# Kernel optimization log

Hardware: AMD Instinct MI355X
Metric: run time of the kernel (lower is better)

Reference implementation:

```python
import jax, jax.numpy as jnp
import numpy as np

N_EMB = 512
EMB_DIM = 64
DECAY = 0.99
EPS = 1e-5


def setup_inputs() -> dict:
    key = jax.random.key(0)
    k1, k2 = jax.random.split(key)
    x = jax.random.normal(k1, (32, EMB_DIM, 64, 64), dtype=jnp.float32)
    weight = jax.random.uniform(k2, (EMB_DIM, N_EMB), dtype=jnp.float32)  # rd_init=True: torch.rand(emb_dim, n_emb)
    cluster_size = jnp.zeros((N_EMB,), dtype=jnp.float32)
    embed_avg = weight  # buffer initialized as embed.clone()
    return {"x": x, "weight": weight, "cluster_size": cluster_size, "embed_avg": embed_avg}


def reference(x, weight, cluster_size, embed_avg):
    B, D, H, W = x.shape
    n_emb = weight.shape[1]
    # (B, D, H, W) -> (N, D) tokens
    flat = jnp.transpose(x, (0, 2, 3, 1)).reshape(-1, D)
    dist = (jnp.sum(flat * flat, axis=1, keepdims=True)
            - 2.0 * (flat @ weight)
            + jnp.sum(weight * weight, axis=0)[None, :])
    argmin = jnp.argmin(dist, axis=1)                      # (N,)
    quant = jnp.take(weight.T, argmin, axis=0)             # gather -> (N, D)
    result = jnp.transpose(quant.reshape(B, H, W, D), (0, 3, 1, 2))  # (B, D, H, W)

    # --- EMA codebook update (training branch) ---
    ones = jnp.ones(argmin.shape, dtype=x.dtype)
    n_idx = jax.ops.segment_sum(ones, argmin, num_segments=n_emb)    # onehot.sum(0)
    n_idx = jnp.where(n_idx == 0, jnp.ones_like(n_idx), n_idx)       # clamp empty clusters to 1
    new_cluster_size = DECAY * cluster_size + (1.0 - DECAY) * n_idx
    embed_sum = jax.ops.segment_sum(flat, argmin, num_segments=n_emb).T  # flatten.T @ onehot -> (D, n_emb)
    new_embed_avg = DECAY * embed_avg + (1.0 - DECAY) * embed_sum
    n = jnp.sum(new_cluster_size)
    cs = (new_cluster_size + EPS) / (n + n_emb * EPS) * n
    new_weight = new_embed_avg / cs[None, :]

    return result, argmin.reshape(B, H, W), new_weight, new_cluster_size, new_embed_avg
```

## Files before the change

### kernel.cpp

```cpp
#include <hip/hip_runtime.h>

#define NEMB 512
#define EMB 64
#define BSTR 262144
#define DECAYF 0.99f
#define OMDF 0.01f
#define EPSF 1e-5f
#define GAP_T 0.012f
#define QCAP 32768

typedef __attribute__((ext_vector_type(8))) short bf16x8;
typedef __attribute__((ext_vector_type(4))) float f32x4;

__device__ __forceinline__ unsigned short f2bf(float f) {
    unsigned u = __float_as_uint(f);
    return (unsigned short)((u + 0x7FFFu + ((u >> 16) & 1u)) >> 16);
}
__device__ __forceinline__ float bf2f(unsigned short h) {
    return __uint_as_float(((unsigned)h) << 16);
}

__global__ void prep_kernel(const float* __restrict__ w,
                            unsigned short* __restrict__ wh, unsigned short* __restrict__ wl,
                            float* __restrict__ wsq,
                            float* __restrict__ cnt_ws, unsigned* __restrict__ gcnt) {
    int j = threadIdx.x;
    if (blockIdx.x < 8) {
        int d0 = blockIdx.x << 3;
        bf16x8 hb, lb;
#pragma unroll
        for (int i = 0; i < 8; ++i) {
            float v = w[(d0 + i) * NEMB + j];
            unsigned short h = f2bf(v);
            hb[i] = (short)h;
            lb[i] = (short)f2bf(v - bf2f(h));
        }
        *(bf16x8*)(wh + j * EMB + d0) = hb;
        *(bf16x8*)(wl + j * EMB + d0) = lb;
    } else {
        float s = 0.f;
#pragma unroll
        for (int d = 0; d < EMB; ++d) { float v = w[d * NEMB + j]; s = fmaf(v, v, s); }
        wsq[j] = s;
        cnt_ws[j] = 0.f;
        if (j == 0) *gcnt = 0u;
    }
}

#define UPD(S1, J1, S2, J2, s_, j_) do { \
    if (s_ < S1 || (s_ == S1 && j_ < J1)) { S2 = S1; J2 = J1; S1 = s_; J1 = j_; } \
    else if (s_ < S2 || (s_ == S2 && j_ < J2)) { S2 = s_; J2 = j_; } } while (0)

__global__ __launch_bounds__(512, 4) void vq_main(
    const float* __restrict__ x,
    const unsigned short* __restrict__ wh, const unsigned short* __restrict__ wl,
    const float* __restrict__ wsq,
    float* __restrict__ out_arg, unsigned* __restrict__ gcnt, int* __restrict__ queue)
{
    __shared__ __align__(16) unsigned char ubuf[65536];
    __shared__ float wsq_s[NEMB];
    __shared__ float xsq_s[256];

    float* xt = (float*)ubuf;
    unsigned short* whs = (unsigned short*)ubuf;
    unsigned short* wls = whs + 16384;

    const int tid = threadIdx.x;
    const int blk = blockIdx.x;
    const int b    = blk >> 4;
    const int hgrp = blk & 15;
    const int t0 = b * 4096 + hgrp * 256;
    const float* xbase = x + b * BSTR + hgrp * 256;

#pragma unroll
    for (int it = 0; it < 8; ++it) {
        int idx = tid + (it << 9);
        int d = idx >> 6, q = idx & 63;
        *(float4*)(xt + d * 256 + (q << 2)) = *(const float4*)(xbase + d * 4096 + (q << 2));
    }
    wsq_s[tid] = wsq[tid];
    __syncthreads();

    if (tid < 256) {
        float s = 0.f;
#pragma unroll
        for (int d = 0; d < EMB; ++d) { float v = xt[d * 256 + tid]; s = fmaf(v, v, s); }
        xsq_s[tid] = s;
    }

    const int lane = tid & 63;
    const int wave = tid >> 6;
    const int l15  = lane & 15;
    const int quad = lane >> 4;
    const int wbase = wave << 5;

    bf16x8 ah[2][2], al[2][2];
#pragma unroll
    for (int mt = 0; mt < 2; ++mt) {
        int m = wbase + (mt << 4) + l15;
#pragma unroll
        for (int ks = 0; ks < 2; ++ks) {
            int k0 = (ks << 5) + (quad << 3);
            bf16x8 hh, ll;
#pragma unroll
            for (int i = 0; i < 8; ++i) {
                float v = xt[(k0 + i) * 256 + m];
                unsigned short h = f2bf(v);
                hh[i] = (short)h;
                ll[i] = (short)f2bf(v - bf2f(h));
            }
            ah[mt][ks] = hh; al[mt][ks] = ll;
        }
    }
    __syncthreads();

    float xq[2][4];
#pragma unroll
    for (int mt = 0; mt < 2; ++mt)
#pragma unroll
        for (int r = 0; r < 4; ++r)
            xq[mt][r] = xsq_s[wbase + (mt << 4) + (quad << 2) + r];

    float v1[2][4], v2[2][4];
    int   j1[2][4];
#pragma unroll
    for (int mt = 0; mt < 2; ++mt)
#pragma unroll
        for (int r = 0; r < 4; ++r) { v1[mt][r] = 3.4e38f; v2[mt][r] = 3.4e38f; j1[mt][r] = 0; }

    const int m7 = l15 & 7;
    const int s0off = ((quad ^ m7) << 3);
    const int s1off = (((4 | quad) ^ m7) << 3);

    for (int half = 0; half < 2; ++half) {
#pragma unroll
        for (int it = 0; it < 8; ++it) {
            int e = tid + (it << 9);
            int arr  = e >> 11;
            int win  = e & 2047;
            int row  = win >> 3;
            int slot = win & 7;
            const unsigned short* src =
                (arr ? wl : wh) + ((half << 8) + row) * EMB + (slot << 3);
            bf16x8 v = *(const bf16x8*)src;
            unsigned short* dstb = arr ? wls : whs;
            *(bf16x8*)(dstb + row * EMB + ((slot ^ (row & 7)) << 3)) = v;
        }
        __syncthreads();

        const int nbase = half << 8;
#pragma unroll 2
        for (int it = 0; it < 16; ++it) {
            const int ib = ((it << 4) + l15) << 6;
            bf16x8 b0 = *(const bf16x8*)(whs + ib + s0off);
            bf16x8 b1 = *(const bf16x8*)(whs + ib + s1off);
            bf16x8 b2 = *(const bf16x8*)(wls + ib + s0off);
            bf16x8 b3 = *(const bf16x8*)(wls + ib + s1off);
            const int n = nbase + (it << 4) + l15;
            float wq = wsq_s[n];

            f32x4 acc0 = (f32x4){0.f, 0.f, 0.f, 0.f};
            f32x4 acc1 = (f32x4){0.f, 0.f, 0.f, 0.f};
            acc0 = __builtin_amdgcn_mfma_f32_16x16x32_bf16(ah[0][0], b0, acc0, 0, 0, 0);
            acc1 = __builtin_amdgcn_mfma_f32_16x16x32_bf16(ah[1][0], b0, acc1, 0, 0, 0);
            acc0 = __builtin_amdgcn_mfma_f32_16x16x32_bf16(ah[0][1], b1, acc0, 0, 0, 0);
            acc1 = __builtin_amdgcn_mfma_f32_16x16x32_bf16(ah[1][1], b1, acc1, 0, 0, 0);
            acc0 = __builtin_amdgcn_mfma_f32_16x16x32_bf16(ah[0][0], b2, acc0, 0, 0, 0);
            acc1 = __builtin_amdgcn_mfma_f32_16x16x32_bf16(ah[1][0], b2, acc1, 0, 0, 0);
            acc0 = __builtin_amdgcn_mfma_f32_16x16x32_bf16(ah[0][1], b3, acc0, 0, 0, 0);
            acc1 = __builtin_amdgcn_mfma_f32_16x16x32_bf16(ah[1][1], b3, acc1, 0, 0, 0);
            acc0 = __builtin_amdgcn_mfma_f32_16x16x32_bf16(al[0][0], b0, acc0, 0, 0, 0);
            acc1 = __builtin_amdgcn_mfma_f32_16x16x32_bf16(al[1][0], b0, acc1, 0, 0, 0);
            acc0 = __builtin_amdgcn_mfma_f32_16x16x32_bf16(al[0][1], b1, acc0, 0, 0, 0);
            acc1 = __builtin_amdgcn_mfma_f32_16x16x32_bf16(al[1][1], b1, acc1, 0, 0, 0);

#pragma unroll
            for (int r = 0; r < 4; ++r) {
                float s0 = fmaf(-2.f, acc0[r], xq[0][r] + wq);
                bool p0 = s0 < v1[0][r];
                float mx0 = fmaxf(s0, v1[0][r]);
                v1[0][r] = fminf(s0, v1[0][r]);
                v2[0][r] = fminf(v2[0][r], mx0);
                j1[0][r] = p0 ? n : j1[0][r];

                float s1 = fmaf(-2.f, acc1[r], xq[1][r] + wq);
                bool p1 = s1 < v1[1][r];
                float mx1 = fmaxf(s1, v1[1][r]);
                v1[1][r] = fminf(s1, v1[1][r]);
                v2[1][r] = fminf(v2[1][r], mx1);
                j1[1][r] = p1 ? n : j1[1][r];
            }
        }
        __syncthreads();
    }

#pragma unroll
    for (int mt = 0; mt < 2; ++mt)
#pragma unroll
        for (int r = 0; r < 4; ++r) {
            float a1 = v1[mt][r], a2 = v2[mt][r];
            int   aj = j1[mt][r];
#pragma unroll
            for (int msk = 1; msk < 16; msk <<= 1) {
                float o1 = __shfl_xor(a1, msk, 64);
                int   oj = __shfl_xor(aj, msk, 64);
                float o2 = __shfl_xor(a2, msk, 64);
                bool take = (o1 < a1) || (o1 == a1 && oj < aj);
                float mx = fmaxf(a1, o1);
                a2 = fminf(fminf(a2, o2), mx);
                a1 = fminf(a1, o1);
                aj = take ? oj : aj;
            }
            v1[mt][r] = a1; v2[mt][r] = a2; j1[mt][r] = aj;
        }

    if (l15 == 0) {
#pragma unroll
        for (int mt = 0; mt < 2; ++mt)
#pragma unroll
            for (int r = 0; r < 4; ++r) {
                int gt = t0 + wbase + (mt << 4) + (quad << 2) + r;
                out_arg[gt] = (float)j1[mt][r];
                if (v2[mt][r] - v1[mt][r] < GAP_T) {
                    unsigned idx = atomicAdd(gcnt, 1u);
                    if (idx < QCAP) queue[idx] = gt;
                }
            }
    }
}

__global__ __launch_bounds__(256) void refine_kernel(
    const float* __restrict__ x, const float* __restrict__ w,
    const float* __restrict__ wsq, const unsigned* __restrict__ gcnt,
    const int* __restrict__ queue, float* __restrict__ out_arg)
{
    __shared__ float wsq_s[NEMB];
    const int tid = threadIdx.x;
    wsq_s[tid] = wsq[tid];
    wsq_s[tid + 256] = wsq[tid + 256];
    __syncthreads();

    unsigned nfu = *gcnt;
    const int nf = (int)(nfu < (unsigned)QCAP ? nfu : (unsigned)QCAP);
    const int lane = tid & 63;
    const int gw = (blockIdx.x << 2) + (tid >> 6);

    for (int i = gw; i < nf; i += 1024) {
        const int t = queue[i] & 131071;
        const int b = t >> 12, pos = t & 4095;
        float xd = x[b * BSTR + lane * 4096 + pos];
        float xqv = xd * xd;
#pragma unroll
        for (int mk = 1; mk < 64; mk <<= 1) xqv += __shfl_xor(xqv, mk, 64);

        float accv[8];
#pragma unroll
        for (int k = 0; k < 8; ++k) accv[k] = 0.f;
#pragma unroll 4
        for (int d = 0; d < EMB; ++d) {
            float4 wa = *(const float4*)(w + d * NEMB + (lane << 2));
            float4 wb = *(const float4*)(w + d * NEMB + 256 + (lane << 2));
            float xv = __shfl(xd, d, 64);
            accv[0] = fmaf(xv, wa.x, accv[0]);
            accv[1] = fmaf(xv, wa.y, accv[1]);
            accv[2] = fmaf(xv, wa.z, accv[2]);
            accv[3] = fmaf(xv, wa.w, accv[3]);
            accv[4] = fmaf(xv, wb.x, accv[4]);
            accv[5] = fmaf(xv, wb.y, accv[5]);
            accv[6] = fmaf(xv, wb.z, accv[6]);
            accv[7] = fmaf(xv, wb.w, accv[7]);
        }

        float S1 = 3.4e38f, S2 = 3.4e38f; int J1 = 0, J2 = 0;
#pragma unroll
        for (int k = 0; k < 8; ++k) {
            int j = (k < 4) ? ((lane << 2) + k) : (256 + (lane << 2) + k - 4);
            float s = (xqv - 2.f * accv[k]) + wsq_s[j];
            UPD(S1, J1, S2, J2, s, j);
        }
#pragma unroll
        for (int mk = 1; mk < 64; mk <<= 1) {
            float os1 = __shfl_xor(S1, mk, 64); int oj1 = __shfl_xor(J1, mk, 64);
            float os2 = __shfl_xor(S2, mk, 64); int oj2 = __shfl_xor(J2, mk, 64);
            UPD(S1, J1, S2, J2, os1, oj1);
            UPD(S1, J1, S2, J2, os2, oj2);
        }

        int jm = J1;
        if (S2 - S1 < 1e-3f) {
            float w1 = w[lane * NEMB + J1];
            float w2 = w[lane * NEMB + J2];
            double e1 = (double)w1 * (double)w1 - 2.0 * (double)xd * (double)w1;
            double e2 = (double)w2 * (double)w2 - 2.0 * (double)xd * (double)w2;
#pragma unroll
            for (int mk = 1; mk < 64; mk <<= 1) {
                e1 += __shfl_xor(e1, mk, 64);
                e2 += __shfl_xor(e2, mk, 64);
            }
            if (e2 < e1 || (e2 == e1 && J2 < J1)) jm = J2;
        }
        if (lane == 0) out_arg[t] = (float)jm;
    }
}

__global__ __launch_bounds__(512) void es_kernel(
    const float* __restrict__ x, const float* __restrict__ arg,
    float* __restrict__ es_p, float* __restrict__ cnt_ws)
{
    __shared__ unsigned short xh[16384];
    __shared__ unsigned short xl[16384];
    __shared__ int args_s[256];
    __shared__ float cacc[NEMB];

    const int tid = threadIdx.x;
    const int blk = blockIdx.x;
    const int flavor = blk >> 7;
    const int chunk = blk & 127;
    const int b = chunk >> 2;
    const int tpos0 = (chunk & 3) << 10;

    cacc[tid] = 0.f;

    const int lane = tid & 63;
    const int wave = tid >> 6;
    const int l15  = lane & 15;
    const int quad = lane >> 4;
    const int jb   = wave << 5;

    f32x4 acc[4][2];
#pragma unroll
    for (int m = 0; m < 4; ++m)
#pragma unroll
        for (int nc = 0; nc < 2; ++nc) acc[m][nc] = (f32x4){0.f, 0.f, 0.f, 0.f};

    for (int st = 0; st < 4; ++st) {
        const int tpos = tpos0 + (st << 8);
#pragma unroll
        for (int it = 0; it < 8; ++it) {
            int idx = tid + (it << 9);
            int d = idx >> 6, q = idx & 63;
            float4 g = *(const float4*)(x + b * BSTR + d * 4096 + tpos + (q << 2));
            unsigned short h0 = f2bf(g.x), h1 = f2bf(g.y), h2 = f2bf(g.z), h3 = f2bf(g.w);
            unsigned short e0 = f2bf(g.x - bf2f(h0)), e1 = f2bf(g.y - bf2f(h1));
            unsigned short e2 = f2bf(g.z - bf2f(h2)), e3 = f2bf(g.w - bf2f(h3));
            int c = q >> 1, half = q & 1;
            int off = d * 256 + ((c ^ (d & 7)) << 3) + (half << 2);
            ushort4 hv = {h0, h1, h2, h3};
            ushort4 lv = {e0, e1, e2, e3};
            *(ushort4*)(xh + off) = hv;
            *(ushort4*)(xl + off) = lv;
        }
        if (tid < 256) args_s[tid] = ((int)arg[b * 4096 + tpos + tid]) & 511;
        __syncthreads();

        if (flavor == 0 && tid < 256) atomicAdd(&cacc[args_s[tid]], 1.f);

#pragma unroll
        for (int kk = 0; kk < 8; ++kk) {
            bf16x8 ah[4], al[4];
#pragma unroll
            for (int m = 0; m < 4; ++m) {
                int d = (m << 4) + l15;
                int coff = ((((kk << 2) + quad) ^ (d & 7)) << 3);
                ah[m] = *(const bf16x8*)(xh + d * 256 + coff);
                al[m] = *(const bf16x8*)(xl + d * 256 + coff);
            }
            int argv[8];
            const int kb = (kk << 5) + (quad << 3);
#pragma unroll
            for (int i = 0; i < 8; ++i) argv[i] = args_s[kb + i];
#pragma unroll
            for (int nc = 0; nc < 2; ++nc) {
                const int jg = (flavor << 8) + jb + (nc << 4) + l15;
                bf16x8 bf;
#pragma unroll
                for (int i = 0; i < 8; ++i) bf[i] = (argv[i] == jg) ? (short)0x3F80 : (short)0;
#pragma unroll
                for (int m = 0; m < 4; ++m) {
                    acc[m][nc] = __builtin_amdgcn_mfma_f32_16x16x32_bf16(ah[m], bf, acc[m][nc], 0, 0, 0);
                    acc[m][nc] = __builtin_amdgcn_mfma_f32_16x16x32_bf16(al[m], bf, acc[m][nc], 0, 0, 0);
                }
            }
        }
        __syncthreads();
    }

    float* ep = es_p + blk * 16384;
#pragma unroll
    for (int m = 0; m < 4; ++m)
#pragma unroll
        for (int nc = 0; nc < 2; ++nc) {
            const int jl = jb + (nc << 4) + l15;
#pragma unroll
            for (int r = 0; r < 4; ++r) {
                const int d = (m << 4) + (quad << 2) + r;
                ep[d * 256 + jl] = acc[m][nc][r];
            }
        }
    if (flavor == 0) {
        float v = cacc[tid];
        if (v != 0.f) atomicAdd(&cnt_ws[tid], v);
    }
}

__global__ __launch_bounds__(256) void finalize_kernel(
    const float* __restrict__ cs_in, const float* __restrict__ avg_in,
    const float* __restrict__ cnt_ws, const float* __restrict__ es_p,
    float* __restrict__ out_w, float* __restrict__ out_ncs,
    float* __restrict__ out_avg) {
    __shared__ float red[256];
    const int tid = threadIdx.x;
    const int d  = blockIdx.x >> 1;
    const int jh = blockIdx.x & 1;

    float c0 = cnt_ws[tid], c1 = cnt_ws[tid + 256];
    float ncs0 = DECAYF * cs_in[tid] + OMDF * ((c0 == 0.f) ? 1.f : c0);
    float ncs1 = DECAYF * cs_in[tid + 256] + OMDF * ((c1 == 0.f) ? 1.f : c1);
    red[tid] = ncs0 + ncs1;
    __syncthreads();
    for (int s = 128; s > 0; s >>= 1) {
        if (tid < s) red[tid] += red[tid + s];
        __syncthreads();
    }
    const float n = red[0];

    const float* ep = es_p + (jh << 7) * 16384 + d * 256 + tid;
    float s = 0.f;
#pragma unroll 16
    for (int c = 0; c < 128; ++c) s += ep[c * 16384];

    const float ncs = jh ? ncs1 : ncs0;
    const float csj = (ncs + EPSF) / (n + (float)NEMB * EPSF) * n;
    const int o = d * NEMB + (jh << 8) + tid;
    const float navg = DECAYF * avg_in[o] + OMDF * s;
    out_avg[o] = navg;
    out_w[o] = navg / csj;
    if (blockIdx.x == 0) { out_ncs[tid] = ncs0; out_ncs[tid + 256] = ncs1; }
}

__global__ __launch_bounds__(512) void result_kernel(
    const float* __restrict__ w, const float* __restrict__ arg,
    float* __restrict__ out_result)
{
    __shared__ float wrow8[8 * 512];
    const int tid = threadIdx.x;
    const int grp = blockIdx.x >> 6;
    const int chunk = blockIdx.x & 63;
#pragma unroll
    for (int d = 0; d < 8; ++d)
        wrow8[(d << 9) + tid] = w[((grp << 3) + d) * NEMB + tid];
    __syncthreads();

    const int t = (chunk << 11) + (tid << 2);
    const int o = (t >> 12) * BSTR + (t & 4095);
    float4 a4 = *(const float4*)(arg + t);
    int j0 = ((int)a4.x) & 511, j1 = ((int)a4.y) & 511;
    int j2 = ((int)a4.z) & 511, j3 = ((int)a4.w) & 511;
#pragma unroll
    for (int d = 0; d < 8; ++d) {
        const int dg = (grp << 3) + d;
        float4 r4 = {wrow8[(d << 9) + j0], wrow8[(d << 9) + j1],
                     wrow8[(d << 9) + j2], wrow8[(d << 9) + j3]};
        *(float4*)(out_result + o + dg * 4096) = r4;
    }
}

extern "C" void kernel_launch(void* const* d_in, const int* in_sizes, int n_in,
                              void* d_out, int out_size, void* d_ws, size_t ws_size,
                              hipStream_t stream) {
    (void)in_sizes; (void)n_in; (void)out_size; (void)ws_size;
    const float* x   = (const float*)d_in[0];
    const float* w   = (const float*)d_in[1];
    const float* cs  = (const float*)d_in[2];
    const float* avg = (const float*)d_in[3];

    float* out = (float*)d_out;
    float* out_result = out;
    float* out_arg    = out + 8388608;
    float* out_w      = out + 8519680;
    float* out_ncs    = out + 8552448;
    float* out_avg    = out + 8552960;
    float* es_p       = out;

    char* wsb = (char*)d_ws;
    unsigned short* wh = (unsigned short*)wsb;
    unsigned short* wl = (unsigned short*)(wsb + 65536);
    float* wsq      = (float*)(wsb + 131072);
    float* cnt_ws   = (float*)(wsb + 133120);
    unsigned* gcnt  = (unsigned*)(wsb + 135168);
    int* queue      = (int*)(wsb + 135232);

    prep_kernel<<<9, 512, 0, stream>>>(w, wh, wl, wsq, cnt_ws, gcnt);
    vq_main<<<512, 512, 0, stream>>>(x, wh, wl, wsq, out_arg, gcnt, queue);
    refine_kernel<<<256, 256, 0, stream>>>(x, w, wsq, gcnt, queue, out_arg);
    es_kernel<<<256, 512, 0, stream>>>(x, out_arg, es_p, cnt_ws);
    finalize_kernel<<<128, 256, 0, stream>>>(cs, avg, cnt_ws, es_p, out_w, out_ncs, out_avg);
    result_kernel<<<512, 512, 0, stream>>>(w, out_arg, out_result);
}
```

Baseline: 182.5 us.

## Drop bf16 low-part in embed-sum, prefetch codebook to registers, widen es grid

In vq_main, the codebook halves are prefetched into registers so their global loads overlap the x tile load. The per-token squared norm is now computed inside the split-to-bf16 loop and reduced with shuffles, which removes a shared-memory pass and a buffer. es_kernel keeps only the high bf16 part of x, which halves its LDS use and MFMA count, and runs twice as many blocks over half the tokens each. finalize is updated to sum 256 partials instead of 128. The refine gap threshold is also halved so fewer tokens are re-checked. Both accuracy changes risk the embed-sum and argmin tie handling going outside tolerance.

```diff
diff --git a/kernel.cpp b/kernel.cpp
--- a/kernel.cpp
+++ b/kernel.cpp
@@ -6,7 +6,7 @@
 #define DECAYF 0.99f
 #define OMDF 0.01f
 #define EPSF 1e-5f
-#define GAP_T 0.012f
+#define GAP_T 0.006f
 #define QCAP 32768
 
 typedef __attribute__((ext_vector_type(8))) short bf16x8;
@@ -59,7 +59,6 @@
 {
     __shared__ __align__(16) unsigned char ubuf[65536];
     __shared__ float wsq_s[NEMB];
-    __shared__ float xsq_s[256];
 
     float* xt = (float*)ubuf;
     unsigned short* whs = (unsigned short*)ubuf;
@@ -72,21 +71,30 @@
     const int t0 = b * 4096 + hgrp * 256;
     const float* xbase = x + b * BSTR + hgrp * 256;
 
+    float4 xreg[8];
 #pragma unroll
     for (int it = 0; it < 8; ++it) {
         int idx = tid + (it << 9);
         int d = idx >> 6, q = idx & 63;
-        *(float4*)(xt + d * 256 + (q << 2)) = *(const float4*)(xbase + d * 4096 + (q << 2));
+        xreg[it] = *(const float4*)(xbase + d * 4096 + (q << 2));
+    }
+    const int slot = tid & 7;
+    const int rowb = tid >> 3;
+    bf16x8 cb[8];
+#pragma unroll
+    for (int it = 0; it < 8; ++it) {
+        int row = rowb + ((it & 3) << 6);
+        const unsigned short* src = (it < 4 ? wh : wl) + row * EMB + (slot << 3);
+        cb[it] = *(const bf16x8*)src;
+    }
+#pragma unroll
+    for (int it = 0; it < 8; ++it) {
+        int idx = tid + (it << 9);
+        int d = idx >> 6, q = idx & 63;
+        *(float4*)(xt + d * 256 + (q << 2)) = xreg[it];
     }
     wsq_s[tid] = wsq[tid];
     __syncthreads();
-
-    if (tid < 256) {
-        float s = 0.f;
-#pragma unroll
-        for (int d = 0; d < EMB; ++d) { float v = xt[d * 256 + tid]; s = fmaf(v, v, s); }
-        xsq_s[tid] = s;
-    }
 
     const int lane = tid & 63;
     const int wave = tid >> 6;
@@ -95,9 +103,11 @@
     const int wbase = wave << 5;
 
     bf16x8 ah[2][2], al[2][2];
+    float xq[2][4];
 #pragma unroll
     for (int mt = 0; mt < 2; ++mt) {
         int m = wbase + (mt << 4) + l15;
+        float sq = 0.f;
 #pragma unroll
         for (int ks = 0; ks < 2; ++ks) {
             int k0 = (ks << 5) + (quad << 3);
@@ -105,21 +115,20 @@
 #pragma unroll
             for (int i = 0; i < 8; ++i) {
                 float v = xt[(k0 + i) * 256 + m];
+                sq = fmaf(v, v, sq);
                 unsigned short h = f2bf(v);
                 hh[i] = (short)h;
                 ll[i] = (short)f2bf(v - bf2f(h));
             }
             ah[mt][ks] = hh; al[mt][ks] = ll;
         }
+        sq += __shfl_xor(sq, 16, 64);
+        sq += __shfl_xor(sq, 32, 64);
+#pragma unroll
+        for (int r = 0; r < 4; ++r)
+            xq[mt][r] = __shfl(sq, (quad << 2) + r, 64);
     }
     __syncthreads();
-
-    float xq[2][4];
-#pragma unroll
-    for (int mt = 0; mt < 2; ++mt)
-#pragma unroll
-        for (int r = 0; r < 4; ++r)
-            xq[mt][r] = xsq_s[wbase + (mt << 4) + (quad << 2) + r];
 
     float v1[2][4], v2[2][4];
     int   j1[2][4];
@@ -135,16 +144,17 @@
     for (int half = 0; half < 2; ++half) {
 #pragma unroll
         for (int it = 0; it < 8; ++it) {
-            int e = tid + (it << 9);
-            int arr  = e >> 11;
-            int win  = e & 2047;
-            int row  = win >> 3;
-            int slot = win & 7;
-            const unsigned short* src =
-                (arr ? wl : wh) + ((half << 8) + row) * EMB + (slot << 3);
-            bf16x8 v = *(const bf16x8*)src;
-            unsigned short* dstb = arr ? wls : whs;
-            *(bf16x8*)(dstb + row * EMB + ((slot ^ (row & 7)) << 3)) = v;
+            int row = rowb + ((it & 3) << 6);
+            unsigned short* dstb = (it < 4) ? whs : wls;
+            *(bf16x8*)(dstb + row * EMB + ((slot ^ (row & 7)) << 3)) = cb[it];
+        }
+        if (half == 0) {
+#pragma unroll
+            for (int it = 0; it < 8; ++it) {
+                int row = rowb + ((it & 3) << 6);
+                const unsigned short* src = (it < 4 ? wh : wl) + (256 + row) * EMB + (slot << 3);
+                cb[it] = *(const bf16x8*)src;
+            }
         }
         __syncthreads();
 
@@ -303,21 +313,20 @@
     }
 }
 
-__global__ __launch_bounds__(512) void es_kernel(
+__global__ __launch_bounds__(512, 4) void es_kernel(
     const float* __restrict__ x, const float* __restrict__ arg,
     float* __restrict__ es_p, float* __restrict__ cnt_ws)
 {
     __shared__ unsigned short xh[16384];
-    __shared__ unsigned short xl[16384];
     __shared__ int args_s[256];
     __shared__ float cacc[NEMB];
 
     const int tid = threadIdx.x;
     const int blk = blockIdx.x;
-    const int flavor = blk >> 7;
-    const int chunk = blk & 127;
-    const int b = chunk >> 2;
-    const int tpos0 = (chunk & 3) << 10;
+    const int flavor = blk & 1;
+    const int chunk  = blk >> 1;
+    const int b = chunk >> 3;
+    const int tpos0 = (chunk & 7) << 9;
 
     cacc[tid] = 0.f;
 
@@ -333,22 +342,17 @@
 #pragma unroll
         for (int nc = 0; nc < 2; ++nc) acc[m][nc] = (f32x4){0.f, 0.f, 0.f, 0.f};
 
-    for (int st = 0; st < 4; ++st) {
+    for (int st = 0; st < 2; ++st) {
         const int tpos = tpos0 + (st << 8);
 #pragma unroll
         for (int it = 0; it < 8; ++it) {
             int idx = tid + (it << 9);
             int d = idx >> 6, q = idx & 63;
             float4 g = *(const float4*)(x + b * BSTR + d * 4096 + tpos + (q << 2));
-            unsigned short h0 = f2bf(g.x), h1 = f2bf(g.y), h2 = f2bf(g.z), h3 = f2bf(g.w);
-            unsigned short e0 = f2bf(g.x - bf2f(h0)), e1 = f2bf(g.y - bf2f(h1));
-            unsigned short e2 = f2bf(g.z - bf2f(h2)), e3 = f2bf(g.w - bf2f(h3));
             int c = q >> 1, half = q & 1;
             int off = d * 256 + ((c ^ (d & 7)) << 3) + (half << 2);
-            ushort4 hv = {h0, h1, h2, h3};
-            ushort4 lv = {e0, e1, e2, e3};
+            ushort4 hv = {f2bf(g.x), f2bf(g.y), f2bf(g.z), f2bf(g.w)};
             *(ushort4*)(xh + off) = hv;
-            *(ushort4*)(xl + off) = lv;
         }
         if (tid < 256) args_s[tid] = ((int)arg[b * 4096 + tpos + tid]) & 511;
         __syncthreads();
@@ -357,13 +361,12 @@
 
 #pragma unroll
         for (int kk = 0; kk < 8; ++kk) {
-            bf16x8 ah[4], al[4];
+            bf16x8 a_[4];
 #pragma unroll
             for (int m = 0; m < 4; ++m) {
                 int d = (m << 4) + l15;
                 int coff = ((((kk << 2) + quad) ^ (d & 7)) << 3);
-                ah[m] = *(const bf16x8*)(xh + d * 256 + coff);
-                al[m] = *(const bf16x8*)(xl + d * 256 + coff);
+                a_[m] = *(const bf16x8*)(xh + d * 256 + coff);
             }
             int argv[8];
             const int kb = (kk << 5) + (quad << 3);
@@ -376,10 +379,8 @@
 #pragma unroll
                 for (int i = 0; i < 8; ++i) bf[i] = (argv[i] == jg) ? (short)0x3F80 : (short)0;
 #pragma unroll
-                for (int m = 0; m < 4; ++m) {
-                    acc[m][nc] = __builtin_amdgcn_mfma_f32_16x16x32_bf16(ah[m], bf, acc[m][nc], 0, 0, 0);
-                    acc[m][nc] = __builtin_amdgcn_mfma_f32_16x16x32_bf16(al[m], bf, acc[m][nc], 0, 0, 0);
-                }
+                for (int m = 0; m < 4; ++m)
+                    acc[m][nc] = __builtin_amdgcn_mfma_f32_16x16x32_bf16(a_[m], bf, acc[m][nc], 0, 0, 0);
             }
         }
         __syncthreads();
@@ -424,10 +425,10 @@
     }
     const float n = red[0];
 
-    const float* ep = es_p + (jh << 7) * 16384 + d * 256 + tid;
+    const float* ep = es_p + jh * 16384 + d * 256 + tid;
     float s = 0.f;
 #pragma unroll 16
-    for (int c = 0; c < 128; ++c) s += ep[c * 16384];
+    for (int c = 0; c < 256; ++c) s += ep[c * 32768];
 
     const float ncs = jh ? ncs1 : ncs0;
     const float csj = (ncs + EPSF) / (n + (float)NEMB * EPSF) * n;
@@ -493,7 +494,7 @@
     prep_kernel<<<9, 512, 0, stream>>>(w, wh, wl, wsq, cnt_ws, gcnt);
     vq_main<<<512, 512, 0, stream>>>(x, wh, wl, wsq, out_arg, gcnt, queue);
     refine_kernel<<<256, 256, 0, stream>>>(x, w, wsq, gcnt, queue, out_arg);
-    es_kernel<<<256, 512, 0, stream>>>(x, out_arg, es_p, cnt_ws);
+    es_kernel<<<512, 512, 0, stream>>>(x, out_arg, es_p, cnt_ws);
     finalize_kernel<<<128, 256, 0, stream>>>(cs, avg, cnt_ws, es_p, out_w, out_ncs, out_avg);
     result_kernel<<<512, 512, 0, stream>>>(w, out_arg, out_result);
 }
```

Result: slower. 187.4 us (+2.7%).
